# Optimization experiments

Hardware: AMD Instinct MI355X
Metric: run time of the kernel (lower is better)

Reference implementation:

```python
import jax, jax.numpy as jnp
import numpy as np
from jax import lax

V, D, H = 32000, 512, 512  # vocab, embedding_dim, hidden_size (must match for the DxD matmul chain)
B, T, A = 64, 256, 4       # batch, sentence len, aspect len
EPS = 1e-5


def setup_inputs() -> dict:
    key = jax.random.key(0)
    ks = jax.random.split(key, 12)
    sc = 0.05
    return {
        "x": jax.random.randint(ks[0], (B, T), 0, V),
        "s": jax.random.randint(ks[1], (B, A), 0, V),
        "embed": jax.random.normal(ks[2], (V, D), jnp.float32) * sc,
        "W_ih": jax.random.normal(ks[3], (4 * H, D), jnp.float32) * sc,
        "W_hh": jax.random.normal(ks[4], (4 * H, H), jnp.float32) * sc,
        "b_lstm": jax.random.normal(ks[5], (4 * H,), jnp.float32) * sc,
        "w_y": jax.random.normal(ks[6], (D, D), jnp.float32) * sc,
        "w_t": jax.random.normal(ks[7], (D, D), jnp.float32) * sc,
        "w_p": jax.random.normal(ks[8], (D, D), jnp.float32) * sc,
        "w_x": jax.random.normal(ks[9], (D, D), jnp.float32) * sc,
        "w_f": jax.random.normal(ks[10], (D, D), jnp.float32) * sc,
        "b_f": jax.random.normal(ks[11], (D,), jnp.float32) * sc,
    }


def _lstm(emb, W_ih, W_hh, b):
    # emb: [B, T, D] -> hidden states [B, T, H]; PyTorch gate order i,f,g,o
    Bx = emb.shape[0]
    Hh = W_hh.shape[1]
    h0 = jnp.zeros((Bx, Hh), emb.dtype)
    c0 = jnp.zeros((Bx, Hh), emb.dtype)

    def step(carry, x_t):
        h, c = carry
        z = x_t @ W_ih.T + h @ W_hh.T + b  # [B, 4H]
        i, f, g, o = jnp.split(z, 4, axis=-1)
        c = jax.nn.sigmoid(f) * c + jax.nn.sigmoid(i) * jnp.tanh(g)
        h = jax.nn.sigmoid(o) * jnp.tanh(c)
        return (h, c), h

    _, hs = lax.scan(step, (h0, c0), jnp.swapaxes(emb, 0, 1))
    return jnp.swapaxes(hs, 0, 1)  # [B, T, H]


def reference(x, s, embed, W_ih, W_hh, b_lstm, w_y, w_t, w_p, w_x, w_f, b_f):
    # 1) embed + LSTM over the sentence
    emb = embed[x]                      # [B, T, D]
    Hs = _lstm(emb, W_ih, W_hh, b_lstm)  # [B, T, H]

    # 2) aspect: embed, batch-normalize per feature, sum over aspect tokens
    s_emb = embed[s]                    # [B, A, D]
    mu = s_emb.mean(axis=(0, 1))
    var = s_emb.var(axis=(0, 1))
    s_norm = ((s_emb - mu) * lax.rsqrt(var + EPS)).sum(axis=1)  # [B, D]

    # 3) FFT circular correlation: m_t = ifft(fft(h_t) * conj(fft(s))).real
    Hf = jnp.fft.fft(Hs, axis=-1)                      # [B, T, D] complex
    Sf = jnp.conj(jnp.fft.fft(s_norm, axis=-1))        # [B, D]
    m = jnp.fft.ifft(Hf * Sf[:, None, :], axis=-1).real.astype(Hs.dtype)  # [B, T, D]

    # 4) attention chain
    Y = jnp.tanh(jnp.einsum('de,bte->btd', w_y, m))            # [B, T, D]
    alpha = jax.nn.softmax(jnp.einsum('de,bte->btd', w_t, Y), axis=1)  # softmax over time
    r = jnp.einsum('btd,btd->bd', alpha, Hs)                   # [B, D]
    h_star = jnp.tanh(r @ w_p.T + Hs[:, -1] @ w_x.T)           # [B, D]
    return jax.nn.softmax(h_star @ w_f.T + b_f, axis=-1)       # [B, D]
```

## Files before the change

kernel.cpp:

```cpp
#include <hip/hip_runtime.h>


typedef __bf16 bf16x8 __attribute__((ext_vector_type(8)));
typedef float f32x4 __attribute__((ext_vector_type(4)));

#define B_ 64
#define T_ 256
#define D_ 512
#define H4 2048

__device__ __forceinline__ unsigned short f2bf(float f) {
    unsigned u = __float_as_uint(f);
    u += 0x7fffu + ((u >> 16) & 1u);
    return (unsigned short)(u >> 16);
}
__device__ __forceinline__ float bf2f(unsigned short x) {
    return __uint_as_float(((unsigned)x) << 16);
}
__device__ __forceinline__ float bf2f_lo(unsigned u) { return __uint_as_float(u << 16); }
__device__ __forceinline__ float bf2f_hi(unsigned u) { return __uint_as_float(u & 0xffff0000u); }

__device__ __forceinline__ float frcp(float x) { return __builtin_amdgcn_rcpf(x); }
__device__ __forceinline__ float fast_sigmoid(float x) {
    return frcp(1.f + __expf(-x));
}
__device__ __forceinline__ float fast_tanh(float x) {
    return 1.f - 2.f * frcp(1.f + __expf(2.f * x));
}

__global__ __launch_bounds__(256)
void fill_sentinel(uint4* __restrict__ dst)
{
    const int i = (blockIdx.x * 256 + threadIdx.x) * 2;
    uint4 v = {0xFFFFFFFFu, 0xFFFFFFFFu, 0xFFFFFFFFu, 0xFFFFFFFFu};
    dst[i] = v;
    dst[i + 1] = v;
}

__global__ __launch_bounds__(256)
void conv_weights(const float* __restrict__ Wih,
                  const float* __restrict__ wy,
                  const float* __restrict__ wt,
                  unsigned short* __restrict__ dst)
{
    const int i = (blockIdx.x * 256 + threadIdx.x) * 4;
    const float* src; int off;
    if (i < 1048576)      { src = Wih; off = 0; }
    else if (i < 1310720) { src = wy;  off = 1048576; }
    else                  { src = wt;  off = 1310720; }
    float4 v = *(const float4*)(src + (i - off));
    unsigned short o[4] __attribute__((aligned(8)));
    o[0] = f2bf(v.x); o[1] = f2bf(v.y); o[2] = f2bf(v.z); o[3] = f2bf(v.w);
    *(unsigned long long*)(dst + i) = *(const unsigned long long*)o;
}

__global__ __launch_bounds__(256)
void conv_embed(const int* __restrict__ x,
                const float* __restrict__ embed,
                unsigned short* __restrict__ Ebf)
{
    const long i = ((long)blockIdx.x * 256 + threadIdx.x) * 8;
    const int row = (int)(i >> 9);
    const int col = (int)(i & 511);
    const float* src = embed + (long)x[row] * 512 + col;
    float4 u0 = *(const float4*)(src);
    float4 u1 = *(const float4*)(src + 4);
    unsigned short o[8] __attribute__((aligned(16)));
    o[0] = f2bf(u0.x); o[1] = f2bf(u0.y); o[2] = f2bf(u0.z); o[3] = f2bf(u0.w);
    o[4] = f2bf(u1.x); o[5] = f2bf(u1.y); o[6] = f2bf(u1.z); o[7] = f2bf(u1.w);
    *(uint4*)(Ebf + i) = *(const uint4*)o;
}

__global__ __launch_bounds__(256)
void gemm_bt(const void* __restrict__ Abase, int a_f32,
             const int* __restrict__ gather_idx,
             const unsigned short* __restrict__ Bmat_h,
             const float* __restrict__ circ_src,
             const float* __restrict__ bias,
             unsigned short* __restrict__ outb,
             float* __restrict__ outf,
             int N, int K,
             long A_bstride, long out_bstride,
             int act)
{
    __shared__ __align__(16) unsigned short Asm[128 * 40];
    __shared__ __align__(16) unsigned short Bsm[128 * 40];

    const int bz = blockIdx.z;
    const int tile_n = blockIdx.x * 128;
    const int tile_m = blockIdx.y * 128;
    const int tid = threadIdx.x;
    const int lane = tid & 63;
    const int w = tid >> 6;
    const int wm = (w >> 1) * 64;
    const int wn = (w & 1) * 64;

    const int srow = tid >> 1;
    const int skc = (tid & 1) * 16;

    const float* arow_f = nullptr;
    const unsigned short* arow_h = nullptr;
    if (a_f32) {
        const float* Af = (const float*)Abase;
        if (gather_idx) arow_f = Af + (long)gather_idx[tile_m + srow] * K;
        else            arow_f = Af + (long)bz * A_bstride + (long)(tile_m + srow) * K;
    } else {
        arow_h = (const unsigned short*)Abase + (long)bz * A_bstride + (long)(tile_m + srow) * K;
    }
    const unsigned short* brow_h = nullptr;
    const float* csrc = nullptr;
    if (circ_src) csrc = circ_src + bz * 512;
    else brow_h = Bmat_h + (long)(tile_n + srow) * K;

    f32x4 zero4 = {0.f, 0.f, 0.f, 0.f};
    f32x4 acc[4][4];
    #pragma unroll
    for (int mi = 0; mi < 4; mi++)
        #pragma unroll
        for (int ni = 0; ni < 4; ni++) acc[mi][ni] = zero4;

    const int fr = lane & 15;
    const int fq = (lane >> 4) * 8;

    for (int kc = 0; kc < K; kc += 32) {
        __syncthreads();
        if (a_f32) {
            float4 u0 = *(const float4*)(arow_f + kc + skc);
            float4 u1 = *(const float4*)(arow_f + kc + skc + 4);
            float4 u2 = *(const float4*)(arow_f + kc + skc + 8);
            float4 u3 = *(const float4*)(arow_f + kc + skc + 12);
            unsigned short tmp[16] __attribute__((aligned(16)));
            tmp[0] = f2bf(u0.x); tmp[1] = f2bf(u0.y); tmp[2]  = f2bf(u0.z); tmp[3]  = f2bf(u0.w);
            tmp[4] = f2bf(u1.x); tmp[5] = f2bf(u1.y); tmp[6]  = f2bf(u1.z); tmp[7]  = f2bf(u1.w);
            tmp[8] = f2bf(u2.x); tmp[9] = f2bf(u2.y); tmp[10] = f2bf(u2.z); tmp[11] = f2bf(u2.w);
            tmp[12] = f2bf(u3.x); tmp[13] = f2bf(u3.y); tmp[14] = f2bf(u3.z); tmp[15] = f2bf(u3.w);
            *(uint4*)&Asm[srow * 40 + skc]     = *(const uint4*)tmp;
            *(uint4*)&Asm[srow * 40 + skc + 8] = *(const uint4*)(tmp + 8);
        } else {
            *(uint4*)&Asm[srow * 40 + skc]     = *(const uint4*)(arow_h + kc + skc);
            *(uint4*)&Asm[srow * 40 + skc + 8] = *(const uint4*)(arow_h + kc + skc + 8);
        }
        if (csrc) {
            unsigned short tmp[16] __attribute__((aligned(16)));
            int n_abs = tile_n + srow;
            #pragma unroll
            for (int j = 0; j < 16; j++) {
                int k_abs = kc + skc + j;
                tmp[j] = f2bf(csrc[(k_abs - n_abs) & 511]);
            }
            *(uint4*)&Bsm[srow * 40 + skc]     = *(const uint4*)tmp;
            *(uint4*)&Bsm[srow * 40 + skc + 8] = *(const uint4*)(tmp + 8);
        } else {
            *(uint4*)&Bsm[srow * 40 + skc]     = *(const uint4*)(brow_h + kc + skc);
            *(uint4*)&Bsm[srow * 40 + skc + 8] = *(const uint4*)(brow_h + kc + skc + 8);
        }
        __syncthreads();
        bf16x8 av[4], bv[4];
        #pragma unroll
        for (int mi = 0; mi < 4; mi++)
            av[mi] = *(const bf16x8*)&Asm[(wm + mi * 16 + fr) * 40 + fq];
        #pragma unroll
        for (int ni = 0; ni < 4; ni++)
            bv[ni] = *(const bf16x8*)&Bsm[(wn + ni * 16 + fr) * 40 + fq];
        #pragma unroll
        for (int mi = 0; mi < 4; mi++)
            #pragma unroll
            for (int ni = 0; ni < 4; ni++)
                acc[mi][ni] = __builtin_amdgcn_mfma_f32_16x16x32_bf16(
                    av[mi], bv[ni], acc[mi][ni], 0, 0, 0);
    }

    #pragma unroll
    for (int mi = 0; mi < 4; mi++) {
        #pragma unroll
        for (int ni = 0; ni < 4; ni++) {
            #pragma unroll
            for (int rg = 0; rg < 4; rg++) {
                int row = tile_m + wm + mi * 16 + (lane >> 4) * 4 + rg;
                int col = tile_n + wn + ni * 16 + (lane & 15);
                float v = acc[mi][ni][rg];
                if (bias) v += bias[col];
                if (act == 1) v = fast_tanh(v);
                long oidx = (long)bz * out_bstride + (long)row * N + col;
                if (outb) outb[oidx] = f2bf(v);
                else outf[oidx] = v;
            }
        }
    }
}

#define WSTRIDE 520
#define SENT 0xFFFFFFFFu
#define ZL(g,r,d) zl[((g)*8+(r))*65+(d)]

__global__ __launch_bounds__(512, 2)
void persistent_lstm(const float* __restrict__ Whh,
                     const unsigned short* __restrict__ Zx,
                     unsigned int* __restrict__ Hsu)
{
    __shared__ __align__(16) unsigned short hsm[16 * WSTRIDE];
    __shared__ float zl[4 * 8 * 65];

    const int cq  = blockIdx.x & 7;
    const int nbp = blockIdx.x >> 3;
    const int tid = threadIdx.x;
    const int w = tid >> 6;
    const int lane = tid & 63;
    const int fr = lane & 15;
    const int fq = (lane >> 4) * 8;
    const int g = w >> 1;
    const int f = w & 1;

    bf16x8 wfrag[2][16];
    #pragma unroll
    for (int n = 0; n < 2; n++) {
        const float* wrow = Whh + (long)(g * 512 + nbp * 64 + f * 32 + n * 16 + fr) * 512;
        #pragma unroll
        for (int c = 0; c < 16; c++) {
            int k0 = c * 32 + fq;
            float4 u0 = *(const float4*)(wrow + k0);
            float4 u1 = *(const float4*)(wrow + k0 + 4);
            unsigned short tmp[8] __attribute__((aligned(16)));
            tmp[0] = f2bf(u0.x); tmp[1] = f2bf(u0.y); tmp[2] = f2bf(u0.z); tmp[3] = f2bf(u0.w);
            tmp[4] = f2bf(u1.x); tmp[5] = f2bf(u1.y); tmp[6] = f2bf(u1.z); tmp[7] = f2bf(u1.w);
            wfrag[n][c] = *(const bf16x8*)tmp;
        }
    }

    for (int i = tid; i < 16 * WSTRIDE / 2; i += 512)
        ((unsigned*)hsm)[i] = 0;

    int st_r[4], st_dp[4];
    #pragma unroll
    for (int k = 0; k < 4; k++) {
        int idx = k * 512 + tid;
        st_r[k] = idx >> 8;
        st_dp[k] = idx & 255;
    }

    const int grow = (tid & 255) >> 5;
    const int d0 = (tid & 31) * 2;
    const int b_own = cq * 8 + grow;
    const int dg = nbp * 64 + d0;
    float ca = 0.f, cb = 0.f;

    f32x4 zero4 = {0.f, 0.f, 0.f, 0.f};

    for (int t = 0; t < T_; t++) {
        unsigned zi_u = 0, zf_u = 0, zg_u = 0, zo_u = 0;
        if (tid < 256) {
            const long zb = ((long)b_own * T_ + t) * H4 + dg;
            zi_u = *(const unsigned*)&Zx[zb + 0 * 512];
            zf_u = *(const unsigned*)&Zx[zb + 1 * 512];
            zg_u = *(const unsigned*)&Zx[zb + 2 * 512];
            zo_u = *(const unsigned*)&Zx[zb + 3 * 512];
        }

        f32x4 an0 = zero4, an1 = zero4;
        if (t > 0) {
            unsigned vv[4];
            long ad[4];
            #pragma unroll
            for (int k = 0; k < 4; k++) {
                ad[k] = ((long)(cq * 8 + st_r[k]) * T_ + (t - 1)) * 256 + st_dp[k];
                vv[k] = __hip_atomic_load(Hsu + ad[k], __ATOMIC_RELAXED,
                                          __HIP_MEMORY_SCOPE_AGENT);
            }
            while (true) {
                bool pend = false;
                #pragma unroll
                for (int k = 0; k < 4; k++) pend |= (vv[k] == SENT);
                if (!__ballot(pend)) break;
                #pragma unroll
                for (int k = 0; k < 4; k++) {
                    vv[k] = __hip_atomic_load(Hsu + ad[k], __ATOMIC_RELAXED,
                                              __HIP_MEMORY_SCOPE_AGENT);
                }
            }
            #pragma unroll
            for (int k = 0; k < 4; k++) {
                *(unsigned*)&hsm[st_r[k] * WSTRIDE + st_dp[k] * 2] = vv[k];
            }
            __syncthreads();
            const unsigned short* arow = hsm + fr * WSTRIDE;
            f32x4 a0[4] = {zero4, zero4, zero4, zero4};
            f32x4 a1[4] = {zero4, zero4, zero4, zero4};
            #pragma unroll
            for (int c = 0; c < 16; c += 4) {
                bf16x8 x0 = *(const bf16x8*)(arow + (c + 0) * 32 + fq);
                bf16x8 x1 = *(const bf16x8*)(arow + (c + 1) * 32 + fq);
                bf16x8 x2 = *(const bf16x8*)(arow + (c + 2) * 32 + fq);
                bf16x8 x3 = *(const bf16x8*)(arow + (c + 3) * 32 + fq);
                a0[0] = __builtin_amdgcn_mfma_f32_16x16x32_bf16(x0, wfrag[0][c + 0], a0[0], 0, 0, 0);
                a0[1] = __builtin_amdgcn_mfma_f32_16x16x32_bf16(x1, wfrag[0][c + 1], a0[1], 0, 0, 0);
                a0[2] = __builtin_amdgcn_mfma_f32_16x16x32_bf16(x2, wfrag[0][c + 2], a0[2], 0, 0, 0);
                a0[3] = __builtin_amdgcn_mfma_f32_16x16x32_bf16(x3, wfrag[0][c + 3], a0[3], 0, 0, 0);
                a1[0] = __builtin_amdgcn_mfma_f32_16x16x32_bf16(x0, wfrag[1][c + 0], a1[0], 0, 0, 0);
                a1[1] = __builtin_amdgcn_mfma_f32_16x16x32_bf16(x1, wfrag[1][c + 1], a1[1], 0, 0, 0);
                a1[2] = __builtin_amdgcn_mfma_f32_16x16x32_bf16(x2, wfrag[1][c + 2], a1[2], 0, 0, 0);
                a1[3] = __builtin_amdgcn_mfma_f32_16x16x32_bf16(x3, wfrag[1][c + 3], a1[3], 0, 0, 0);
            }
            an0 = (a0[0] + a0[1]) + (a0[2] + a0[3]);
            an1 = (a1[0] + a1[1]) + (a1[2] + a1[3]);
        }
        if (lane < 32) {
            const int rb = (lane >> 4) * 4;
            const int cl = f * 32 + (lane & 15);
            #pragma unroll
            for (int rg = 0; rg < 4; rg++) {
                ZL(g, rb + rg, cl)      = an0[rg];
                ZL(g, rb + rg, cl + 16) = an1[rg];
            }
        }
        __syncthreads();
        if (tid < 256) {
            float zi0 = ZL(0, grow, d0)     + bf2f_lo(zi_u);
            float zi1 = ZL(0, grow, d0 + 1) + bf2f_hi(zi_u);
            float zf0 = ZL(1, grow, d0)     + bf2f_lo(zf_u);
            float zf1 = ZL(1, grow, d0 + 1) + bf2f_hi(zf_u);
            float zg0 = ZL(2, grow, d0)     + bf2f_lo(zg_u);
            float zg1 = ZL(2, grow, d0 + 1) + bf2f_hi(zg_u);
            float zo0 = ZL(3, grow, d0)     + bf2f_lo(zo_u);
            float zo1 = ZL(3, grow, d0 + 1) + bf2f_hi(zo_u);

            ca = fast_sigmoid(zf0) * ca + fast_sigmoid(zi0) * fast_tanh(zg0);
            cb = fast_sigmoid(zf1) * cb + fast_sigmoid(zi1) * fast_tanh(zg1);
            float h0 = fast_sigmoid(zo0) * fast_tanh(ca);
            float h1 = fast_sigmoid(zo1) * fast_tanh(cb);

            unsigned hp = (unsigned)f2bf(h0) | ((unsigned)f2bf(h1) << 16);
            __hip_atomic_store(Hsu + ((long)b_own * T_ + t) * 256 + nbp * 32 + (tid & 31),
                               hp, __ATOMIC_RELAXED, __HIP_MEMORY_SCOPE_AGENT);
        }
    }
}

__global__ __launch_bounds__(64)
void aspect_norm(const int* __restrict__ s,
                 const float* __restrict__ embed,
                 float* __restrict__ s_norm)
{
    __shared__ int sidx[256];
    const int tid = threadIdx.x;
    const int d = blockIdx.x * 64 + tid;
    for (int i = tid; i < 256; i += 64) sidx[i] = s[i];
    __syncthreads();
    float sum = 0.f, sq = 0.f;
    for (int i = 0; i < 256; i++) {
        float v = embed[(long)sidx[i] * D_ + d];
        sum += v; sq += v * v;
    }
    float mu = sum * (1.f / 256.f);
    float var = sq * (1.f / 256.f) - mu * mu;
    float rstd = rsqrtf(var + 1e-5f);
    for (int b = 0; b < 64; b++) {
        float acc = 0.f;
        #pragma unroll
        for (int a = 0; a < 4; a++) {
            acc += embed[(long)sidx[b * 4 + a] * D_ + d] - mu;
        }
        s_norm[b * D_ + d] = acc * rstd;
    }
}

__global__ __launch_bounds__(256)
void attn_r(const float* __restrict__ apre,
            const unsigned short* __restrict__ Hs,
            float* __restrict__ r)
{
    const int b = blockIdx.y;
    const int d = blockIdx.x * 256 + threadIdx.x;
    const float* ap = apre + (long)b * T_ * D_ + d;
    const unsigned short* hp = Hs + (long)b * T_ * D_ + d;
    float mx = ap[0], sm = 1.f;
    for (int t = 1; t < T_; t++) {
        float v = ap[(long)t * D_];
        if (v > mx) { sm = sm * __expf(mx - v) + 1.f; mx = v; }
        else sm += __expf(v - mx);
    }
    float acc = 0.f;
    for (int t = 0; t < T_; t++) {
        acc += __expf(ap[(long)t * D_] - mx) * bf2f(hp[(long)t * D_]);
    }
    r[b * D_ + d] = acc / sm;
}

__global__ __launch_bounds__(256)
void hstar_kernel(const float* __restrict__ r,
                  const unsigned short* __restrict__ Hs,
                  const float* __restrict__ w_p,
                  const float* __restrict__ w_x,
                  float* __restrict__ h_star)
{
    __shared__ float rs[512];
    __shared__ float hts[512];
    const int b = blockIdx.x, tid = threadIdx.x;
    const long hlast = ((long)b * T_ + (T_ - 1)) * D_;
    rs[tid] = r[b * D_ + tid];
    rs[tid + 256] = r[b * D_ + 256 + tid];
    hts[tid] = bf2f(Hs[hlast + tid]);
    hts[tid + 256] = bf2f(Hs[hlast + 256 + tid]);
    __syncthreads();
    for (int d = tid; d < 512; d += 256) {
        const float* wp = w_p + (long)d * D_;
        const float* wx = w_x + (long)d * D_;
        float acc = 0.f;
        for (int e = 0; e < 512; e += 4) {
            float4 p1 = *(const float4*)(wp + e);
            float4 p2 = *(const float4*)(wx + e);
            acc += p1.x * rs[e] + p1.y * rs[e + 1] + p1.z * rs[e + 2] + p1.w * rs[e + 3];
            acc += p2.x * hts[e] + p2.y * hts[e + 1] + p2.z * hts[e + 2] + p2.w * hts[e + 3];
        }
        h_star[b * D_ + d] = fast_tanh(acc);
    }
}

__global__ __launch_bounds__(256)
void out_kernel(const float* __restrict__ h_star,
                const float* __restrict__ w_f,
                const float* __restrict__ b_f,
                float* __restrict__ out)
{
    __shared__ float hs[512];
    __shared__ float lg[512];
    __shared__ float red[8];
    const int b = blockIdx.x, tid = threadIdx.x;
    hs[tid] = h_star[b * D_ + tid];
    hs[tid + 256] = h_star[b * D_ + 256 + tid];
    __syncthreads();
    for (int d = tid; d < 512; d += 256) {
        const float* wr = w_f + (long)d * D_;
        float acc = b_f[d];
        for (int e = 0; e < 512; e += 4) {
            float4 p = *(const float4*)(wr + e);
            acc += p.x * hs[e] + p.y * hs[e + 1] + p.z * hs[e + 2] + p.w * hs[e + 3];
        }
        lg[d] = acc;
    }
    __syncthreads();
    float m0 = fmaxf(lg[tid], lg[tid + 256]);
    for (int off = 32; off > 0; off >>= 1) m0 = fmaxf(m0, __shfl_down(m0, off, 64));
    if ((tid & 63) == 0) red[tid >> 6] = m0;
    __syncthreads();
    float bmax = fmaxf(fmaxf(red[0], red[1]), fmaxf(red[2], red[3]));
    float e0 = __expf(lg[tid] - bmax);
    float e1 = __expf(lg[tid + 256] - bmax);
    float s0 = e0 + e1;
    for (int off = 32; off > 0; off >>= 1) s0 += __shfl_down(s0, off, 64);
    if ((tid & 63) == 0) red[4 + (tid >> 6)] = s0;
    __syncthreads();
    float inv = 1.f / (red[4] + red[5] + red[6] + red[7]);
    out[b * D_ + tid] = e0 * inv;
    out[b * D_ + 256 + tid] = e1 * inv;
}

extern "C" void kernel_launch(void* const* d_in, const int* in_sizes, int n_in,
                              void* d_out, int out_size, void* d_ws, size_t ws_size,
                              hipStream_t stream)
{
    (void)in_sizes; (void)n_in; (void)out_size;

    const int* x = (const int*)d_in[0];
    const int* s = (const int*)d_in[1];
    const float* embed  = (const float*)d_in[2];
    const float* W_ih   = (const float*)d_in[3];
    const float* W_hh   = (const float*)d_in[4];
    const float* b_lstm = (const float*)d_in[5];
    const float* w_y = (const float*)d_in[6];
    const float* w_t = (const float*)d_in[7];
    const float* w_p = (const float*)d_in[8];
    const float* w_x = (const float*)d_in[9];
    const float* w_f = (const float*)d_in[10];
    const float* b_f = (const float*)d_in[11];

    char* ws = (char*)d_ws;
    unsigned short* Zx   = (unsigned short*)(ws + 0);
    float*          apre = (float*)(ws + 0);
    unsigned short* mbuf = (unsigned short*)(ws + 33554432);
    unsigned short* Ybuf = (unsigned short*)(ws + 50331648);
    unsigned short* Hs   = (unsigned short*)(ws + 67108864);
    float* s_norm = (float*)(ws + 86114304);
    float* rbuf   = (float*)(ws + 86245376);
    float* hstar  = (float*)(ws + 86376448);
    unsigned short* Wcat = (unsigned short*)(ws + 86507520);
    unsigned short* Wih_bf = Wcat;
    unsigned short* wy_bf  = Wcat + 1048576;
    unsigned short* wt_bf  = Wcat + 1310720;
    unsigned short* Ebf  = (unsigned short*)(ws + 89653248);
    const int use_ebf = (ws_size >= (size_t)89653248 + 16777216u);

    fill_sentinel<<<dim3(2048), dim3(256), 0, stream>>>((uint4*)Hs);

    conv_weights<<<dim3(1536), dim3(256), 0, stream>>>(W_ih, w_y, w_t, Wcat);

    if (use_ebf)
        conv_embed<<<dim3(4096), dim3(256), 0, stream>>>(x, embed, Ebf);

    aspect_norm<<<dim3(8), dim3(64), 0, stream>>>(s, embed, s_norm);

    if (use_ebf)
        gemm_bt<<<dim3(16, 128, 1), dim3(256), 0, stream>>>(
            Ebf, 0, nullptr, Wih_bf, nullptr, b_lstm, Zx, nullptr,
            2048, 512, 0L, 0L, 0);
    else
        gemm_bt<<<dim3(16, 128, 1), dim3(256), 0, stream>>>(
            embed, 1, x, Wih_bf, nullptr, b_lstm, Zx, nullptr,
            2048, 512, 0L, 0L, 0);

    persistent_lstm<<<dim3(64), dim3(512), 0, stream>>>(
        W_hh, Zx, (unsigned int*)Hs);


    gemm_bt<<<dim3(4, 2, 64), dim3(256), 0, stream>>>(
        Hs, 0, nullptr, nullptr, s_norm, nullptr, mbuf, nullptr,
        512, 512, (long)(T_ * D_), (long)(T_ * D_), 0);

    gemm_bt<<<dim3(4, 128, 1), dim3(256), 0, stream>>>(
        mbuf, 0, nullptr, wy_bf, nullptr, nullptr, Ybuf, nullptr,
        512, 512, 0L, 0L, 1);

    gemm_bt<<<dim3(4, 128, 1), dim3(256), 0, stream>>>(
        Ybuf, 0, nullptr, wt_bf, nullptr, nullptr, nullptr, apre,
        512, 512, 0L, 0L, 0);

    attn_r<<<dim3(2, 64), dim3(256), 0, stream>>>(apre, Hs, rbuf);

    hstar_kernel<<<dim3(64), dim3(256), 0, stream>>>(rbuf, Hs, w_p, w_x, hstar);

    out_kernel<<<dim3(64), dim3(256), 0, stream>>>(hstar, w_f, b_f, (float*)d_out);
}
```

Baseline: 1.009 ms.

## Fuse prep kernels into one launch and merge attention tail kernels

The four preprocessing kernels (sentinel fill, weight conversion, embedding gather/convert, aspect normalisation) are merged into one launch that dispatches on block index. The attention-pooling, h_star and output-softmax kernels are fused into a single per-batch tail kernel. That kernel uses a one-pass online softmax, staging apre and Hs tiles through shared memory. This removes several launches and intermediate round-trips, but the tail now runs on only 64 blocks instead of 128 for the reduction phase.

```diff
diff --git a/kernel.cpp b/kernel.cpp
--- a/kernel.cpp
+++ b/kernel.cpp
@@ -29,46 +29,70 @@
 }
 
 __global__ __launch_bounds__(256)
-void fill_sentinel(uint4* __restrict__ dst)
+void prep_kernel(const int* __restrict__ x,
+                 const int* __restrict__ s,
+                 const float* __restrict__ embed,
+                 const float* __restrict__ Wih,
+                 const float* __restrict__ wy,
+                 const float* __restrict__ wt,
+                 unsigned short* __restrict__ Wcat,
+                 unsigned short* __restrict__ Ebf,
+                 uint4* __restrict__ Hs4,
+                 float* __restrict__ s_norm,
+                 int use_ebf)
 {
-    const int i = (blockIdx.x * 256 + threadIdx.x) * 2;
-    uint4 v = {0xFFFFFFFFu, 0xFFFFFFFFu, 0xFFFFFFFFu, 0xFFFFFFFFu};
-    dst[i] = v;
-    dst[i + 1] = v;
-}
-
-__global__ __launch_bounds__(256)
-void conv_weights(const float* __restrict__ Wih,
-                  const float* __restrict__ wy,
-                  const float* __restrict__ wt,
-                  unsigned short* __restrict__ dst)
-{
-    const int i = (blockIdx.x * 256 + threadIdx.x) * 4;
-    const float* src; int off;
-    if (i < 1048576)      { src = Wih; off = 0; }
-    else if (i < 1310720) { src = wy;  off = 1048576; }
-    else                  { src = wt;  off = 1310720; }
-    float4 v = *(const float4*)(src + (i - off));
-    unsigned short o[4] __attribute__((aligned(8)));
-    o[0] = f2bf(v.x); o[1] = f2bf(v.y); o[2] = f2bf(v.z); o[3] = f2bf(v.w);
-    *(unsigned long long*)(dst + i) = *(const unsigned long long*)o;
-}
-
-__global__ __launch_bounds__(256)
-void conv_embed(const int* __restrict__ x,
-                const float* __restrict__ embed,
-                unsigned short* __restrict__ Ebf)
-{
-    const long i = ((long)blockIdx.x * 256 + threadIdx.x) * 8;
-    const int row = (int)(i >> 9);
-    const int col = (int)(i & 511);
-    const float* src = embed + (long)x[row] * 512 + col;
-    float4 u0 = *(const float4*)(src);
-    float4 u1 = *(const float4*)(src + 4);
-    unsigned short o[8] __attribute__((aligned(16)));
-    o[0] = f2bf(u0.x); o[1] = f2bf(u0.y); o[2] = f2bf(u0.z); o[3] = f2bf(u0.w);
-    o[4] = f2bf(u1.x); o[5] = f2bf(u1.y); o[6] = f2bf(u1.z); o[7] = f2bf(u1.w);
-    *(uint4*)(Ebf + i) = *(const uint4*)o;
+    __shared__ int sidx[256];
+    const int bid = blockIdx.x;
+    const int tid = threadIdx.x;
+
+    if (bid < 2048) {
+        const int i = (bid * 256 + tid) * 2;
+        uint4 v = {0xFFFFFFFFu, 0xFFFFFFFFu, 0xFFFFFFFFu, 0xFFFFFFFFu};
+        Hs4[i] = v;
+        Hs4[i + 1] = v;
+    } else if (bid < 3584) {
+        const int i = ((bid - 2048) * 256 + tid) * 4;
+        const float* src; int off;
+        if (i < 1048576)      { src = Wih; off = 0; }
+        else if (i < 1310720) { src = wy;  off = 1048576; }
+        else                  { src = wt;  off = 1310720; }
+        float4 v = *(const float4*)(src + (i - off));
+        unsigned short o[4] __attribute__((aligned(8)));
+        o[0] = f2bf(v.x); o[1] = f2bf(v.y); o[2] = f2bf(v.z); o[3] = f2bf(v.w);
+        *(unsigned long long*)(Wcat + i) = *(const unsigned long long*)o;
+    } else if (bid < 7680) {
+        if (!use_ebf) return;
+        const long i = ((long)(bid - 3584) * 256 + tid) * 8;
+        const int row = (int)(i >> 9);
+        const int col = (int)(i & 511);
+        const float* src = embed + (long)x[row] * 512 + col;
+        float4 u0 = *(const float4*)(src);
+        float4 u1 = *(const float4*)(src + 4);
+        unsigned short o[8] __attribute__((aligned(16)));
+        o[0] = f2bf(u0.x); o[1] = f2bf(u0.y); o[2] = f2bf(u0.z); o[3] = f2bf(u0.w);
+        o[4] = f2bf(u1.x); o[5] = f2bf(u1.y); o[6] = f2bf(u1.z); o[7] = f2bf(u1.w);
+        *(uint4*)(Ebf + i) = *(const uint4*)o;
+    } else {
+        const int d = (bid - 7680) * 256 + tid;
+        sidx[tid] = s[tid];
+        __syncthreads();
+        float sum = 0.f, sq = 0.f;
+        for (int i = 0; i < 256; i++) {
+            float v = embed[(long)sidx[i] * D_ + d];
+            sum += v; sq += v * v;
+        }
+        float mu = sum * (1.f / 256.f);
+        float var = sq * (1.f / 256.f) - mu * mu;
+        float rstd = rsqrtf(var + 1e-5f);
+        for (int b = 0; b < 64; b++) {
+            float acc = 0.f;
+            #pragma unroll
+            for (int a = 0; a < 4; a++) {
+                acc += embed[(long)sidx[b * 4 + a] * D_ + d] - mu;
+            }
+            s_norm[b * D_ + d] = acc * rstd;
+        }
+    }
 }
 
 __global__ __launch_bounds__(256)
@@ -335,72 +359,77 @@
     }
 }
 
-__global__ __launch_bounds__(64)
-void aspect_norm(const int* __restrict__ s,
-                 const float* __restrict__ embed,
-                 float* __restrict__ s_norm)
+__global__ __launch_bounds__(256)
+void tail_kernel(const float* __restrict__ apre,
+                 const unsigned short* __restrict__ Hs,
+                 const float* __restrict__ w_p,
+                 const float* __restrict__ w_x,
+                 const float* __restrict__ w_f,
+                 const float* __restrict__ b_f,
+                 float* __restrict__ out)
 {
-    __shared__ int sidx[256];
-    const int tid = threadIdx.x;
-    const int d = blockIdx.x * 64 + tid;
-    for (int i = tid; i < 256; i += 64) sidx[i] = s[i];
-    __syncthreads();
-    float sum = 0.f, sq = 0.f;
-    for (int i = 0; i < 256; i++) {
-        float v = embed[(long)sidx[i] * D_ + d];
-        sum += v; sq += v * v;
-    }
-    float mu = sum * (1.f / 256.f);
-    float var = sq * (1.f / 256.f) - mu * mu;
-    float rstd = rsqrtf(var + 1e-5f);
-    for (int b = 0; b < 64; b++) {
-        float acc = 0.f;
-        #pragma unroll
-        for (int a = 0; a < 4; a++) {
-            acc += embed[(long)sidx[b * 4 + a] * D_ + d] - mu;
-        }
-        s_norm[b * D_ + d] = acc * rstd;
-    }
-}
-
-__global__ __launch_bounds__(256)
-void attn_r(const float* __restrict__ apre,
-            const unsigned short* __restrict__ Hs,
-            float* __restrict__ r)
-{
-    const int b = blockIdx.y;
-    const int d = blockIdx.x * 256 + threadIdx.x;
-    const float* ap = apre + (long)b * T_ * D_ + d;
-    const unsigned short* hp = Hs + (long)b * T_ * D_ + d;
-    float mx = ap[0], sm = 1.f;
-    for (int t = 1; t < T_; t++) {
-        float v = ap[(long)t * D_];
-        if (v > mx) { sm = sm * __expf(mx - v) + 1.f; mx = v; }
-        else sm += __expf(v - mx);
-    }
-    float acc = 0.f;
-    for (int t = 0; t < T_; t++) {
-        acc += __expf(ap[(long)t * D_] - mx) * bf2f(hp[(long)t * D_]);
-    }
-    r[b * D_ + d] = acc / sm;
-}
-
-__global__ __launch_bounds__(256)
-void hstar_kernel(const float* __restrict__ r,
-                  const unsigned short* __restrict__ Hs,
-                  const float* __restrict__ w_p,
-                  const float* __restrict__ w_x,
-                  float* __restrict__ h_star)
-{
+    __shared__ __align__(16) float apc[16 * 512];
+    __shared__ __align__(16) unsigned short hc[16 * 512];
     __shared__ float rs[512];
     __shared__ float hts[512];
+    __shared__ float hsr[512];
+    __shared__ float lg[512];
+    __shared__ float red[8];
+
     const int b = blockIdx.x, tid = threadIdx.x;
+    const int d1 = tid + 256;
+    const float* apb = apre + (long)b * T_ * D_;
+    const unsigned short* hpb = Hs + (long)b * T_ * D_;
+
+    float mx0 = -3.0e38f, sm0 = 0.f, ac0 = 0.f;
+    float mx1 = -3.0e38f, sm1 = 0.f, ac1 = 0.f;
+
+    for (int t0 = 0; t0 < T_; t0 += 16) {
+        __syncthreads();
+        for (int idx = tid; idx < 16 * 128; idx += 256) {
+            int rr = idx >> 7, cc = (idx & 127) * 4;
+            *(float4*)&apc[rr * 512 + cc] = *(const float4*)(apb + (long)(t0 + rr) * 512 + cc);
+        }
+        for (int idx = tid; idx < 16 * 64; idx += 256) {
+            int rr = idx >> 6, cc = (idx & 63) * 8;
+            *(uint4*)&hc[rr * 512 + cc] = *(const uint4*)(hpb + (long)(t0 + rr) * 512 + cc);
+        }
+        __syncthreads();
+        #pragma unroll
+        for (int i = 0; i < 16; i++) {
+            float v0 = apc[i * 512 + tid];
+            float h0 = bf2f(hc[i * 512 + tid]);
+            if (v0 > mx0) {
+                float fct = __expf(mx0 - v0);
+                sm0 = sm0 * fct + 1.f;
+                ac0 = ac0 * fct + h0;
+                mx0 = v0;
+            } else {
+                float e = __expf(v0 - mx0);
+                sm0 += e;
+                ac0 += e * h0;
+            }
+            float v1 = apc[i * 512 + d1];
+            float h1 = bf2f(hc[i * 512 + d1]);
+            if (v1 > mx1) {
+                float fct = __expf(mx1 - v1);
+                sm1 = sm1 * fct + 1.f;
+                ac1 = ac1 * fct + h1;
+                mx1 = v1;
+            } else {
+                float e = __expf(v1 - mx1);
+                sm1 += e;
+                ac1 += e * h1;
+            }
+        }
+    }
+    rs[tid] = ac0 / sm0;
+    rs[d1]  = ac1 / sm1;
     const long hlast = ((long)b * T_ + (T_ - 1)) * D_;
-    rs[tid] = r[b * D_ + tid];
-    rs[tid + 256] = r[b * D_ + 256 + tid];
     hts[tid] = bf2f(Hs[hlast + tid]);
-    hts[tid + 256] = bf2f(Hs[hlast + 256 + tid]);
+    hts[d1]  = bf2f(Hs[hlast + d1]);
     __syncthreads();
+
     for (int d = tid; d < 512; d += 256) {
         const float* wp = w_p + (long)d * D_;
         const float* wx = w_x + (long)d * D_;
@@ -411,47 +440,34 @@
             acc += p1.x * rs[e] + p1.y * rs[e + 1] + p1.z * rs[e + 2] + p1.w * rs[e + 3];
             acc += p2.x * hts[e] + p2.y * hts[e + 1] + p2.z * hts[e + 2] + p2.w * hts[e + 3];
         }
-        h_star[b * D_ + d] = fast_tanh(acc);
-    }
-}
-
-__global__ __launch_bounds__(256)
-void out_kernel(const float* __restrict__ h_star,
-                const float* __restrict__ w_f,
-                const float* __restrict__ b_f,
-                float* __restrict__ out)
-{
-    __shared__ float hs[512];
-    __shared__ float lg[512];
-    __shared__ float red[8];
-    const int b = blockIdx.x, tid = threadIdx.x;
-    hs[tid] = h_star[b * D_ + tid];
-    hs[tid + 256] = h_star[b * D_ + 256 + tid];
+        hsr[d] = fast_tanh(acc);
+    }
     __syncthreads();
+
     for (int d = tid; d < 512; d += 256) {
         const float* wr = w_f + (long)d * D_;
         float acc = b_f[d];
         for (int e = 0; e < 512; e += 4) {
             float4 p = *(const float4*)(wr + e);
-            acc += p.x * hs[e] + p.y * hs[e + 1] + p.z * hs[e + 2] + p.w * hs[e + 3];
+            acc += p.x * hsr[e] + p.y * hsr[e + 1] + p.z * hsr[e + 2] + p.w * hsr[e + 3];
         }
         lg[d] = acc;
     }
     __syncthreads();
-    float m0 = fmaxf(lg[tid], lg[tid + 256]);
+    float m0 = fmaxf(lg[tid], lg[d1]);
     for (int off = 32; off > 0; off >>= 1) m0 = fmaxf(m0, __shfl_down(m0, off, 64));
     if ((tid & 63) == 0) red[tid >> 6] = m0;
     __syncthreads();
     float bmax = fmaxf(fmaxf(red[0], red[1]), fmaxf(red[2], red[3]));
     float e0 = __expf(lg[tid] - bmax);
-    float e1 = __expf(lg[tid + 256] - bmax);
+    float e1 = __expf(lg[d1] - bmax);
     float s0 = e0 + e1;
     for (int off = 32; off > 0; off >>= 1) s0 += __shfl_down(s0, off, 64);
     if ((tid & 63) == 0) red[4 + (tid >> 6)] = s0;
     __syncthreads();
     float inv = 1.f / (red[4] + red[5] + red[6] + red[7]);
     out[b * D_ + tid] = e0 * inv;
-    out[b * D_ + 256 + tid] = e1 * inv;
+    out[b * D_ + d1]  = e1 * inv;
 }
 
 extern "C" void kernel_launch(void* const* d_in, const int* in_sizes, int n_in,
@@ -480,8 +496,6 @@
     unsigned short* Ybuf = (unsigned short*)(ws + 50331648);
     unsigned short* Hs   = (unsigned short*)(ws + 67108864);
     float* s_norm = (float*)(ws + 86114304);
-    float* rbuf   = (float*)(ws + 86245376);
-    float* hstar  = (float*)(ws + 86376448);
     unsigned short* Wcat = (unsigned short*)(ws + 86507520);
     unsigned short* Wih_bf = Wcat;
     unsigned short* wy_bf  = Wcat + 1048576;
@@ -489,14 +503,8 @@
     unsigned short* Ebf  = (unsigned short*)(ws + 89653248);
     const int use_ebf = (ws_size >= (size_t)89653248 + 16777216u);
 
-    fill_sentinel<<<dim3(2048), dim3(256), 0, stream>>>((uint4*)Hs);
-
-    conv_weights<<<dim3(1536), dim3(256), 0, stream>>>(W_ih, w_y, w_t, Wcat);
-
-    if (use_ebf)
-        conv_embed<<<dim3(4096), dim3(256), 0, stream>>>(x, embed, Ebf);
-
-    aspect_norm<<<dim3(8), dim3(64), 0, stream>>>(s, embed, s_norm);
+    prep_kernel<<<dim3(7682), dim3(256), 0, stream>>>(
+        x, s, embed, W_ih, w_y, w_t, Wcat, Ebf, (uint4*)Hs, s_norm, use_ebf);
 
     if (use_ebf)
         gemm_bt<<<dim3(16, 128, 1), dim3(256), 0, stream>>>(
@@ -523,9 +531,6 @@
         Ybuf, 0, nullptr, wt_bf, nullptr, nullptr, nullptr, apre,
         512, 512, 0L, 0L, 0);
 
-    attn_r<<<dim3(2, 64), dim3(256), 0, stream>>>(apre, Hs, rbuf);
-
-    hstar_kernel<<<dim3(64), dim3(256), 0, stream>>>(rbuf, Hs, w_p, w_x, hstar);
-
-    out_kernel<<<dim3(64), dim3(256), 0, stream>>>(hstar, w_f, b_f, (float*)d_out);
-}
+    tail_kernel<<<dim3(64), dim3(256), 0, stream>>>(
+        apre, Hs, w_p, w_x, w_f, b_f, (float*)d_out);
+}
```

Result: faster. 967.7 us (-4.1%).
